# Optimization experiments

Measured on AMD Instinct MI355X. Metric: run time of the kernel, lower is better.

Reference implementation:

```python
import jax, jax.numpy as jnp
import numpy as np

C_IN = 64
C_INT = 32

def conv1x1(x, w, b):
    # x: [B,C,H,W], w: [O,C], b: [O]
    return jnp.einsum('bchw,oc->bohw', x, w) + b[None, :, None, None]

def maxpool2(x):
    # 2x2 max pool, stride 2. x: [B,C,H,W]
    B, C, H, W = x.shape
    return x.reshape(B, C, H // 2, 2, W // 2, 2).max(axis=(3, 5))

def setup_inputs() -> dict:
    key = jax.random.key(0)
    ks = jax.random.split(key, 9)
    s = 1.0 / np.sqrt(C_IN)
    si = 1.0 / np.sqrt(C_INT)
    x = jax.random.normal(ks[0], (16, C_IN, 64, 64), dtype=jnp.float32)
    return {
        'x': x,
        'w_origin': jax.random.normal(ks[1], (C_INT, C_IN), dtype=jnp.float32) * s,
        'b_origin': jax.random.normal(ks[2], (C_INT,), dtype=jnp.float32) * s,
        'w_theta': jax.random.normal(ks[3], (C_INT, C_IN), dtype=jnp.float32) * s,
        'b_theta': jax.random.normal(ks[4], (C_INT,), dtype=jnp.float32) * s,
        'w_phi': jax.random.normal(ks[5], (C_INT, C_IN), dtype=jnp.float32) * s,
        'b_phi': jax.random.normal(ks[6], (C_INT,), dtype=jnp.float32) * s,
        'w_W': jax.random.normal(ks[7], (C_IN, C_INT), dtype=jnp.float32) * si,
        'b_W': jax.random.normal(ks[8], (C_IN,), dtype=jnp.float32) * si,
    }

def reference(x, w_origin, b_origin, w_theta, b_theta, w_phi, b_phi, w_W, b_W):
    B, C, H, W = x.shape
    # value: conv1x1 + maxpool -> [B, Ci, H/2, W/2] -> [B, Nkv, Ci]
    f_x = maxpool2(conv1x1(x, w_origin, b_origin))
    f_x = f_x.reshape(B, C_INT, -1).transpose(0, 2, 1)
    # query: conv1x1 (no pooling) -> [B, N, Ci]
    theta_x = conv1x1(x, w_theta, b_theta).reshape(B, C_INT, -1).transpose(0, 2, 1)
    # key: conv1x1 + maxpool -> [B, Ci, Nkv]
    phi_x = maxpool2(conv1x1(x, w_phi, b_phi)).reshape(B, C_INT, -1)
    # attention: [B, N, Nkv]
    f = jnp.einsum('bnc,bcm->bnm', theta_x, phi_x)
    f_div_C = jax.nn.softmax(f, axis=-1)
    y = jnp.einsum('bnm,bmc->bnc', f_div_C, f_x)  # [B, N, Ci]
    y = y.transpose(0, 2, 1).reshape(B, C_INT, H, W)
    z = conv1x1(y, w_W, b_W) + x
    return z
```

## Files before the change

kernel.cpp:

```cpp
#include <hip/hip_runtime.h>
#include <math.h>


#define B_SZ 16
#define HW 4096
#define NKV 1024
#define XSTR 65
#define YS 40
#define LOG2E 1.4426950408889634f

typedef __attribute__((ext_vector_type(8))) short bfrag;
typedef __attribute__((ext_vector_type(4))) short sfrag;
typedef __attribute__((ext_vector_type(4))) float f32x4;

static __device__ __forceinline__ ushort f2bf(float v) {
  union { float f; uint u; } c; c.f = v;
  uint b = c.u + 0x7FFFu + ((c.u >> 16) & 1u);
  return (ushort)(b >> 16);
}
static __device__ __forceinline__ float bf2f(ushort h) {
  union { uint u; float f; } c; c.u = (uint)h << 16; return c.f;
}

__global__ __launch_bounds__(512) void k_qkv(
    const float* __restrict__ x,
    const float* __restrict__ wt, const float* __restrict__ bt,
    const float* __restrict__ wp, const float* __restrict__ bp,
    const float* __restrict__ wo, const float* __restrict__ bo,
    ushort* __restrict__ QH, ushort* __restrict__ QL,
    ushort* __restrict__ KH, ushort* __restrict__ KL, ushort* __restrict__ VF) {
  __shared__ float sx[128 * XSTR];
  __shared__ float sPool[2][2][32][33];

  int t = threadIdx.x;
  int W = t >> 6, lane = t & 63, l15 = lane & 15, quad = lane >> 4;
  int bb = blockIdx.x >> 5, rg = blockIdx.x & 31;
  int p0 = rg * 128;

  #pragma unroll
  for (int i = 0; i < 4; ++i) {
    int f = i * 512 + t;
    int c = f >> 5, u = f & 31;
    float4 v = *(const float4*)(x + ((size_t)bb << 18) + (size_t)c * HW + p0 + 4 * u);
    sx[(4*u+0) * XSTR + c] = v.x;
    sx[(4*u+1) * XSTR + c] = v.y;
    sx[(4*u+2) * XSTR + c] = v.z;
    sx[(4*u+3) * XSTR + c] = v.w;
  }
  __syncthreads();

  int pix = W * 16 + l15;
  bfrag xh[2], xl[2];
  #pragma unroll
  for (int kh2 = 0; kh2 < 2; ++kh2)
    #pragma unroll
    for (int j = 0; j < 8; ++j) {
      float v = sx[pix * XSTR + kh2 * 32 + quad * 8 + j];
      ushort hb = f2bf(v);
      xh[kh2][j] = (short)hb;
      xl[kh2][j] = (short)f2bf(v - bf2f(hb));
    }
  __syncthreads();

  f32x4 acc[2];

  acc[0] = (f32x4){0.f,0.f,0.f,0.f}; acc[1] = (f32x4){0.f,0.f,0.f,0.f};
  #pragma unroll
  for (int kh2 = 0; kh2 < 2; ++kh2)
    #pragma unroll
    for (int nt = 0; nt < 2; ++nt) {
      bfrag wh, wl;
      const float* wrow = wt + (size_t)(nt * 16 + l15) * 64 + kh2 * 32 + quad * 8;
      #pragma unroll
      for (int j = 0; j < 8; ++j) {
        float v = wrow[j] * LOG2E;
        ushort hb = f2bf(v);
        wh[j] = (short)hb; wl[j] = (short)f2bf(v - bf2f(hb));
      }
      acc[nt] = __builtin_amdgcn_mfma_f32_16x16x32_bf16(xh[kh2], wh, acc[nt], 0, 0, 0);
      acc[nt] = __builtin_amdgcn_mfma_f32_16x16x32_bf16(xl[kh2], wh, acc[nt], 0, 0, 0);
      acc[nt] = __builtin_amdgcn_mfma_f32_16x16x32_bf16(xh[kh2], wl, acc[nt], 0, 0, 0);
    }
  #pragma unroll
  for (int nt = 0; nt < 2; ++nt) {
    float bias = bt[nt * 16 + l15] * LOG2E;
    #pragma unroll
    for (int r = 0; r < 4; ++r)
      sx[(W * 16 + quad * 4 + r) * XSTR + nt * 16 + l15] = acc[nt][r] + bias;
  }

  int prow = (W * 16 + quad * 4) >> 6;
  int px2  = ((W * 16 + quad * 4) & 63) >> 1;

  acc[0] = (f32x4){0.f,0.f,0.f,0.f}; acc[1] = (f32x4){0.f,0.f,0.f,0.f};
  #pragma unroll
  for (int kh2 = 0; kh2 < 2; ++kh2)
    #pragma unroll
    for (int nt = 0; nt < 2; ++nt) {
      bfrag wh, wl;
      const float* wrow = wp + (size_t)(nt * 16 + l15) * 64 + kh2 * 32 + quad * 8;
      #pragma unroll
      for (int j = 0; j < 8; ++j) {
        float v = wrow[j];
        ushort hb = f2bf(v);
        wh[j] = (short)hb; wl[j] = (short)f2bf(v - bf2f(hb));
      }
      acc[nt] = __builtin_amdgcn_mfma_f32_16x16x32_bf16(xh[kh2], wh, acc[nt], 0, 0, 0);
      acc[nt] = __builtin_amdgcn_mfma_f32_16x16x32_bf16(xl[kh2], wh, acc[nt], 0, 0, 0);
      acc[nt] = __builtin_amdgcn_mfma_f32_16x16x32_bf16(xh[kh2], wl, acc[nt], 0, 0, 0);
    }
  #pragma unroll
  for (int nt = 0; nt < 2; ++nt) {
    float bias = bp[nt * 16 + l15];
    sPool[0][prow][px2    ][nt * 16 + l15] = fmaxf(acc[nt][0], acc[nt][1]) + bias;
    sPool[0][prow][px2 + 1][nt * 16 + l15] = fmaxf(acc[nt][2], acc[nt][3]) + bias;
  }

  acc[0] = (f32x4){0.f,0.f,0.f,0.f}; acc[1] = (f32x4){0.f,0.f,0.f,0.f};
  #pragma unroll
  for (int kh2 = 0; kh2 < 2; ++kh2)
    #pragma unroll
    for (int nt = 0; nt < 2; ++nt) {
      bfrag wh;
      const float* wrow = wo + (size_t)(nt * 16 + l15) * 64 + kh2 * 32 + quad * 8;
      #pragma unroll
      for (int j = 0; j < 8; ++j) wh[j] = (short)f2bf(wrow[j]);
      acc[nt] = __builtin_amdgcn_mfma_f32_16x16x32_bf16(xh[kh2], wh, acc[nt], 0, 0, 0);
      acc[nt] = __builtin_amdgcn_mfma_f32_16x16x32_bf16(xl[kh2], wh, acc[nt], 0, 0, 0);
    }
  #pragma unroll
  for (int nt = 0; nt < 2; ++nt) {
    float bias = bo[nt * 16 + l15];
    sPool[1][prow][px2    ][nt * 16 + l15] = fmaxf(acc[nt][0], acc[nt][1]) + bias;
    sPool[1][prow][px2 + 1][nt * 16 + l15] = fmaxf(acc[nt][2], acc[nt][3]) + bias;
  }
  __syncthreads();

  {
    int qt = t >> 6, ln = t & 63, fl = ln & 15, fq = ln >> 4;
    union { ushort u[8]; uint4 v; } Hh, Ll;
    #pragma unroll
    for (int j = 0; j < 8; ++j) {
      float v = sx[(qt * 16 + fl) * XSTR + fq * 8 + j];
      ushort hb = f2bf(v);
      Hh.u[j] = hb;
      Ll.u[j] = f2bf(v - bf2f(hb));
    }
    size_t base = ((size_t)(bb * 256 + rg * 8 + qt) * 64 + ln) * 8;
    *(uint4*)(QH + base) = Hh.v;
    *(uint4*)(QL + base) = Ll.v;
  }

  #pragma unroll
  for (int f = t; f < 1024; f += 512) {
    int tt = f >> 9, rem = f & 511;
    int ln = rem >> 3, j = rem & 7;
    int kvl = tt * 16 + (ln & 15);
    int ch = (ln >> 4) * 8 + j;
    float v = fmaxf(sPool[0][0][kvl][ch], sPool[0][1][kvl][ch]);
    ushort hb = f2bf(v);
    size_t base = ((size_t)(bb * 64 + rg * 2 + tt) * 64 + ln) * 8 + j;
    KH[base] = hb;
    KL[base] = f2bf(v - bf2f(hb));
  }

  #pragma unroll
  for (int f = t; f < 1024; f += 512) {
    int tt = f >> 9, mt = (f >> 8) & 1;
    int ln = (f >> 2) & 63, j = f & 3;
    int kvl = tt * 16 + ((ln >> 4) << 2) + j;
    int ch = mt * 16 + (ln & 15);
    float v = fmaxf(sPool[1][0][kvl][ch], sPool[1][1][kvl][ch]);
    VF[(((size_t)(bb * 64 + rg * 2 + tt) * 2 + mt) * 64 + ln) * 4 + j] = f2bf(v);
  }
}

__global__ __launch_bounds__(256, 4) void k_attn(
    const ushort* __restrict__ QH, const ushort* __restrict__ QL,
    const ushort* __restrict__ KH, const ushort* __restrict__ KL,
    const ushort* __restrict__ VF,
    const float* __restrict__ x, const float* __restrict__ wW,
    const float* __restrict__ bW, float* __restrict__ z) {
  __shared__ float smem[4 * 64 * 36 + 4 * 64];
  float* mrg = smem;
  float* sS  = smem + 4 * 64 * 36;

  int t = threadIdx.x;
  int w = t >> 6, lane = t & 63, l15 = lane & 15, quad = lane >> 4;
  int bb = blockIdx.x >> 6;
  int bq = blockIdx.x & 63;

  bfrag qh[4], ql[4];
  #pragma unroll
  for (int qt = 0; qt < 4; ++qt) {
    size_t base = ((size_t)(bb * 256 + bq * 4 + qt) * 64 + lane) * 8;
    qh[qt] = *(const bfrag*)(QH + base);
    ql[qt] = *(const bfrag*)(QL + base);
  }

  const ushort* KHb = KH + (size_t)bb * 64 * 64 * 8;
  const ushort* KLb = KL + (size_t)bb * 64 * 64 * 8;
  const ushort* VFb = VF + (size_t)bb * 64 * 2 * 64 * 4;

  f32x4 accO[4][2];
  float spart[4] = {0.f, 0.f, 0.f, 0.f};
  #pragma unroll
  for (int qt = 0; qt < 4; ++qt) {
    accO[qt][0] = (f32x4){0.f,0.f,0.f,0.f};
    accO[qt][1] = (f32x4){0.f,0.f,0.f,0.f};
  }

  bfrag kh[2], kl[2];
  sfrag vf[2][2];
  auto loadT = [&](int buf, int i) {
    int gt = w * 16 + i;
    size_t kb = ((size_t)gt * 64 + lane) * 8;
    kh[buf] = *(const bfrag*)(KHb + kb);
    kl[buf] = *(const bfrag*)(KLb + kb);
    vf[buf][0] = *(const sfrag*)(VFb + (((size_t)gt * 2 + 0) * 64 + lane) * 4);
    vf[buf][1] = *(const sfrag*)(VFb + (((size_t)gt * 2 + 1) * 64 + lane) * 4);
  };

  loadT(0, 0);
  #pragma unroll 2
  for (int i = 0; i < 16; ++i) {
    int cur = i & 1;
    if (i < 15) loadT(cur ^ 1, i + 1);
    #pragma unroll
    for (int qt = 0; qt < 4; ++qt) {
      f32x4 s = (f32x4){0.f,0.f,0.f,0.f};
      s = __builtin_amdgcn_mfma_f32_16x16x32_bf16(kh[cur], qh[qt], s, 0, 0, 0);
      s = __builtin_amdgcn_mfma_f32_16x16x32_bf16(kh[cur], ql[qt], s, 0, 0, 0);
      s = __builtin_amdgcn_mfma_f32_16x16x32_bf16(kl[cur], qh[qt], s, 0, 0, 0);
      float e0 = exp2f(s[0]), e1 = exp2f(s[1]);
      float e2 = exp2f(s[2]), e3 = exp2f(s[3]);
      spart[qt] += (e0 + e1) + (e2 + e3);
      union { uint2 u; sfrag s4; } pk;
      pk.u.x = (__float_as_uint(e0) >> 16) | (__float_as_uint(e1) & 0xFFFF0000u);
      pk.u.y = (__float_as_uint(e2) >> 16) | (__float_as_uint(e3) & 0xFFFF0000u);
      accO[qt][0] = __builtin_amdgcn_mfma_f32_16x16x16bf16_1k(vf[cur][0], pk.s4, accO[qt][0], 0, 0, 0);
      accO[qt][1] = __builtin_amdgcn_mfma_f32_16x16x16bf16_1k(vf[cur][1], pk.s4, accO[qt][1], 0, 0, 0);
    }
  }

  #pragma unroll
  for (int qt = 0; qt < 4; ++qt) {
    spart[qt] += __shfl_xor(spart[qt], 16);
    spart[qt] += __shfl_xor(spart[qt], 32);
  }

  #pragma unroll
  for (int qt = 0; qt < 4; ++qt) {
    #pragma unroll
    for (int mt = 0; mt < 2; ++mt)
      *(float4*)&mrg[((size_t)w * 64 + qt * 16 + l15) * 36 + mt * 16 + quad * 4] =
          make_float4(accO[qt][mt][0], accO[qt][mt][1], accO[qt][mt][2], accO[qt][mt][3]);
    if (lane < 16) sS[w * 64 + qt * 16 + l15] = spart[qt];
  }
  __syncthreads();

  int rq = t >> 2, rc = (t & 3) * 8;
  float yv[8];
  {
    float ssum = sS[rq] + sS[64 + rq] + sS[128 + rq] + sS[192 + rq];
    float inv = 1.0f / ssum;
    #pragma unroll
    for (int h = 0; h < 2; ++h) {
      float4 a = *(const float4*)&mrg[(size_t)rq * 36 + rc + 4 * h];
      float4 b = *(const float4*)&mrg[(size_t)(64 + rq) * 36 + rc + 4 * h];
      float4 c = *(const float4*)&mrg[(size_t)(128 + rq) * 36 + rc + 4 * h];
      float4 d = *(const float4*)&mrg[(size_t)(192 + rq) * 36 + rc + 4 * h];
      yv[4*h+0] = (a.x + b.x + c.x + d.x) * inv;
      yv[4*h+1] = (a.y + b.y + c.y + d.y) * inv;
      yv[4*h+2] = (a.z + b.z + c.z + d.z) * inv;
      yv[4*h+3] = (a.w + b.w + c.w + d.w) * inv;
    }
  }
  __syncthreads();

  ushort* yH = (ushort*)mrg;
  ushort* yL = yH + 64 * YS;
  {
    union { ushort u[8]; uint4 v; } Hh, Ll;
    #pragma unroll
    for (int j = 0; j < 8; ++j) {
      ushort hb = f2bf(yv[j]);
      Hh.u[j] = hb;
      Ll.u[j] = f2bf(yv[j] - bf2f(hb));
    }
    *(uint4*)&yH[rq * YS + rc] = Hh.v;
    *(uint4*)&yL[rq * YS + rc] = Ll.v;
  }
  __syncthreads();

  #pragma unroll
  for (int nt = 0; nt < 4; ++nt) {
    f32x4 d = (f32x4){0.f,0.f,0.f,0.f};
    #pragma unroll
    for (int kt = 0; kt < 2; ++kt) {
      float4 w4 = *(const float4*)&wW[(size_t)(w * 16 + l15) * 32 + kt * 16 + quad * 4];
      sfrag ah, al, yhf, ylf;
      #pragma unroll
      for (int j = 0; j < 4; ++j) {
        float v = (&w4.x)[j];
        ushort hb = f2bf(v);
        ah[j] = (short)hb; al[j] = (short)f2bf(v - bf2f(hb));
      }
      yhf = *(const sfrag*)&yH[(nt * 16 + l15) * YS + kt * 16 + quad * 4];
      ylf = *(const sfrag*)&yL[(nt * 16 + l15) * YS + kt * 16 + quad * 4];
      d = __builtin_amdgcn_mfma_f32_16x16x16bf16_1k(ah, yhf, d, 0, 0, 0);
      d = __builtin_amdgcn_mfma_f32_16x16x16bf16_1k(al, yhf, d, 0, 0, 0);
      d = __builtin_amdgcn_mfma_f32_16x16x16bf16_1k(ah, ylf, d, 0, 0, 0);
    }
    #pragma unroll
    for (int r = 0; r < 4; ++r) {
      int cout = w * 16 + quad * 4 + r;
      size_t zi = ((size_t)bb << 18) + ((size_t)cout << 12)
                + (size_t)(bq * 4 + nt) * 16 + l15;
      z[zi] = d[r] + bW[cout] + x[zi];
    }
  }
}

extern "C" void kernel_launch(void* const* d_in, const int* in_sizes, int n_in,
                              void* d_out, int out_size, void* d_ws, size_t ws_size,
                              hipStream_t stream) {
  const float* x   = (const float*)d_in[0];
  const float* w_o = (const float*)d_in[1];
  const float* b_o = (const float*)d_in[2];
  const float* w_t = (const float*)d_in[3];
  const float* b_t = (const float*)d_in[4];
  const float* w_p = (const float*)d_in[5];
  const float* b_p = (const float*)d_in[6];
  const float* w_W = (const float*)d_in[7];
  const float* b_W = (const float*)d_in[8];
  float* z = (float*)d_out;

  ushort* QH = (ushort*)d_ws;
  ushort* QL = QH + 2097152;
  ushort* KH = QL + 2097152;
  ushort* KL = KH + 524288;
  ushort* VF = KL + 524288;

  k_qkv<<<dim3(B_SZ * 32), dim3(512), 0, stream>>>(
      x, w_t, b_t, w_p, b_p, w_o, b_o, QH, QL, KH, KL, VF);
  k_attn<<<dim3(B_SZ * 64), dim3(256), 0, stream>>>(
      QH, QL, KH, KL, VF, x, w_W, b_W, z);
}
```

Before: 128.0 us.

## Fuse projection and attention kernels with per-batch spin barrier, keep Q in LDS

Merges the QKV projection kernel and the attention kernel into one launch. Each block now computes a 64-pixel tile's projections, writes K/V to global memory and keeps Q and the x tile in shared memory. Blocks then wait on a per-batch atomic counter spin barrier before running attention, and the residual add reads x from LDS. This removes the Q global round-trip, the second launch and the residual reload. In exchange it depends on all 64 blocks of a batch being co-resident, which risks deadlock otherwise. It also adds an extra memset and stores the per-wave partial outputs as bf16, which lowers accuracy.

After: 177.6 us. 38.7% more time.

```diff
diff --git a/kernel.cpp b/kernel.cpp
--- a/kernel.cpp
+++ b/kernel.cpp
@@ -4,9 +4,7 @@
 
 #define B_SZ 16
 #define HW 4096
-#define NKV 1024
-#define XSTR 65
-#define YS 40
+#define MST 40
 #define LOG2E 1.4426950408889634f
 
 typedef __attribute__((ext_vector_type(8))) short bfrag;
@@ -22,45 +20,54 @@
   union { uint u; float f; } c; c.u = (uint)h << 16; return c.f;
 }
 
-__global__ __launch_bounds__(512) void k_qkv(
+__global__ __launch_bounds__(256, 4) void k_fused(
     const float* __restrict__ x,
     const float* __restrict__ wt, const float* __restrict__ bt,
     const float* __restrict__ wp, const float* __restrict__ bp,
     const float* __restrict__ wo, const float* __restrict__ bo,
-    ushort* __restrict__ QH, ushort* __restrict__ QL,
-    ushort* __restrict__ KH, ushort* __restrict__ KL, ushort* __restrict__ VF) {
-  __shared__ float sx[128 * XSTR];
-  __shared__ float sPool[2][2][32][33];
+    const float* __restrict__ wW, const float* __restrict__ bW,
+    ushort* __restrict__ KH, ushort* __restrict__ KL, ushort* __restrict__ VF,
+    uint* __restrict__ ctr, float* __restrict__ z) {
+  __shared__ __align__(16) char smem_raw[16640 + 21504];
+  float*  sx    = (float*)smem_raw;
+  char*   reg2  = smem_raw + 16640;
+  float*  sQ    = (float*)reg2;
+  float*  sPool = (float*)(reg2 + 8448);
+  ushort* mrg   = (ushort*)reg2;
+  float*  sS    = (float*)(reg2 + 20480);
+  ushort* yH    = (ushort*)reg2;
+  ushort* yL    = yH + 64 * MST;
 
   int t = threadIdx.x;
-  int W = t >> 6, lane = t & 63, l15 = lane & 15, quad = lane >> 4;
-  int bb = blockIdx.x >> 5, rg = blockIdx.x & 31;
-  int p0 = rg * 128;
+  int w = t >> 6, lane = t & 63, l15 = lane & 15, quad = lane >> 4;
+  int b = blockIdx.x;
+  int bb = b >> 6, s = b & 63, r = s >> 1, j = s & 1;
+  const float* xb = x + ((size_t)bb << 18);
+  int grow0 = 2 * r, gcol0 = 32 * j;
 
   #pragma unroll
   for (int i = 0; i < 4; ++i) {
-    int f = i * 512 + t;
-    int c = f >> 5, u = f & 31;
-    float4 v = *(const float4*)(x + ((size_t)bb << 18) + (size_t)c * HW + p0 + 4 * u);
-    sx[(4*u+0) * XSTR + c] = v.x;
-    sx[(4*u+1) * XSTR + c] = v.y;
-    sx[(4*u+2) * XSTR + c] = v.z;
-    sx[(4*u+3) * XSTR + c] = v.w;
-  }
-  __syncthreads();
-
-  int pix = W * 16 + l15;
+    int f = i * 256 + t;
+    int ch = f >> 4, rem = f & 15, lrow = rem >> 3, c4 = rem & 7;
+    float4 v = *(const float4*)(xb + (size_t)ch * 4096
+                                   + (size_t)(grow0 + lrow) * 64 + gcol0 + c4 * 4);
+    int lp = lrow * 32 + c4 * 4;
+    sx[(lp+0)*65 + ch] = v.x; sx[(lp+1)*65 + ch] = v.y;
+    sx[(lp+2)*65 + ch] = v.z; sx[(lp+3)*65 + ch] = v.w;
+  }
+  __syncthreads();
+
+  int lpix = w * 16 + l15;
   bfrag xh[2], xl[2];
   #pragma unroll
   for (int kh2 = 0; kh2 < 2; ++kh2)
     #pragma unroll
-    for (int j = 0; j < 8; ++j) {
-      float v = sx[pix * XSTR + kh2 * 32 + quad * 8 + j];
+    for (int jj = 0; jj < 8; ++jj) {
+      float v = sx[lpix * 65 + kh2 * 32 + quad * 8 + jj];
       ushort hb = f2bf(v);
-      xh[kh2][j] = (short)hb;
-      xl[kh2][j] = (short)f2bf(v - bf2f(hb));
-    }
-  __syncthreads();
+      xh[kh2][jj] = (short)hb;
+      xl[kh2][jj] = (short)f2bf(v - bf2f(hb));
+    }
 
   f32x4 acc[2];
 
@@ -72,10 +79,10 @@
       bfrag wh, wl;
       const float* wrow = wt + (size_t)(nt * 16 + l15) * 64 + kh2 * 32 + quad * 8;
       #pragma unroll
-      for (int j = 0; j < 8; ++j) {
-        float v = wrow[j] * LOG2E;
+      for (int jj = 0; jj < 8; ++jj) {
+        float v = wrow[jj] * LOG2E;
         ushort hb = f2bf(v);
-        wh[j] = (short)hb; wl[j] = (short)f2bf(v - bf2f(hb));
+        wh[jj] = (short)hb; wl[jj] = (short)f2bf(v - bf2f(hb));
       }
       acc[nt] = __builtin_amdgcn_mfma_f32_16x16x32_bf16(xh[kh2], wh, acc[nt], 0, 0, 0);
       acc[nt] = __builtin_amdgcn_mfma_f32_16x16x32_bf16(xl[kh2], wh, acc[nt], 0, 0, 0);
@@ -85,12 +92,11 @@
   for (int nt = 0; nt < 2; ++nt) {
     float bias = bt[nt * 16 + l15] * LOG2E;
     #pragma unroll
-    for (int r = 0; r < 4; ++r)
-      sx[(W * 16 + quad * 4 + r) * XSTR + nt * 16 + l15] = acc[nt][r] + bias;
-  }
-
-  int prow = (W * 16 + quad * 4) >> 6;
-  int px2  = ((W * 16 + quad * 4) & 63) >> 1;
+    for (int rr = 0; rr < 4; ++rr)
+      sQ[(w * 16 + quad * 4 + rr) * 33 + nt * 16 + l15] = acc[nt][rr] + bias;
+  }
+
+  int hp = w * 8 + quad * 2;
 
   acc[0] = (f32x4){0.f,0.f,0.f,0.f}; acc[1] = (f32x4){0.f,0.f,0.f,0.f};
   #pragma unroll
@@ -100,10 +106,10 @@
       bfrag wh, wl;
       const float* wrow = wp + (size_t)(nt * 16 + l15) * 64 + kh2 * 32 + quad * 8;
       #pragma unroll
-      for (int j = 0; j < 8; ++j) {
-        float v = wrow[j];
+      for (int jj = 0; jj < 8; ++jj) {
+        float v = wrow[jj];
         ushort hb = f2bf(v);
-        wh[j] = (short)hb; wl[j] = (short)f2bf(v - bf2f(hb));
+        wh[jj] = (short)hb; wl[jj] = (short)f2bf(v - bf2f(hb));
       }
       acc[nt] = __builtin_amdgcn_mfma_f32_16x16x32_bf16(xh[kh2], wh, acc[nt], 0, 0, 0);
       acc[nt] = __builtin_amdgcn_mfma_f32_16x16x32_bf16(xl[kh2], wh, acc[nt], 0, 0, 0);
@@ -112,8 +118,8 @@
   #pragma unroll
   for (int nt = 0; nt < 2; ++nt) {
     float bias = bp[nt * 16 + l15];
-    sPool[0][prow][px2    ][nt * 16 + l15] = fmaxf(acc[nt][0], acc[nt][1]) + bias;
-    sPool[0][prow][px2 + 1][nt * 16 + l15] = fmaxf(acc[nt][2], acc[nt][3]) + bias;
+    sPool[(0 * 32 + hp    ) * 33 + nt * 16 + l15] = fmaxf(acc[nt][0], acc[nt][1]) + bias;
+    sPool[(0 * 32 + hp + 1) * 33 + nt * 16 + l15] = fmaxf(acc[nt][2], acc[nt][3]) + bias;
   }
 
   acc[0] = (f32x4){0.f,0.f,0.f,0.f}; acc[1] = (f32x4){0.f,0.f,0.f,0.f};
@@ -124,79 +130,60 @@
       bfrag wh;
       const float* wrow = wo + (size_t)(nt * 16 + l15) * 64 + kh2 * 32 + quad * 8;
       #pragma unroll
-      for (int j = 0; j < 8; ++j) wh[j] = (short)f2bf(wrow[j]);
+      for (int jj = 0; jj < 8; ++jj) wh[jj] = (short)f2bf(wrow[jj]);
       acc[nt] = __builtin_amdgcn_mfma_f32_16x16x32_bf16(xh[kh2], wh, acc[nt], 0, 0, 0);
       acc[nt] = __builtin_amdgcn_mfma_f32_16x16x32_bf16(xl[kh2], wh, acc[nt], 0, 0, 0);
     }
   #pragma unroll
   for (int nt = 0; nt < 2; ++nt) {
     float bias = bo[nt * 16 + l15];
-    sPool[1][prow][px2    ][nt * 16 + l15] = fmaxf(acc[nt][0], acc[nt][1]) + bias;
-    sPool[1][prow][px2 + 1][nt * 16 + l15] = fmaxf(acc[nt][2], acc[nt][3]) + bias;
-  }
-  __syncthreads();
-
-  {
-    int qt = t >> 6, ln = t & 63, fl = ln & 15, fq = ln >> 4;
-    union { ushort u[8]; uint4 v; } Hh, Ll;
-    #pragma unroll
-    for (int j = 0; j < 8; ++j) {
-      float v = sx[(qt * 16 + fl) * XSTR + fq * 8 + j];
-      ushort hb = f2bf(v);
-      Hh.u[j] = hb;
-      Ll.u[j] = f2bf(v - bf2f(hb));
-    }
-    size_t base = ((size_t)(bb * 256 + rg * 8 + qt) * 64 + ln) * 8;
-    *(uint4*)(QH + base) = Hh.v;
-    *(uint4*)(QL + base) = Ll.v;
-  }
-
-  #pragma unroll
-  for (int f = t; f < 1024; f += 512) {
-    int tt = f >> 9, rem = f & 511;
-    int ln = rem >> 3, j = rem & 7;
-    int kvl = tt * 16 + (ln & 15);
-    int ch = (ln >> 4) * 8 + j;
-    float v = fmaxf(sPool[0][0][kvl][ch], sPool[0][1][kvl][ch]);
+    sPool[(1 * 32 + hp    ) * 33 + nt * 16 + l15] = fmaxf(acc[nt][0], acc[nt][1]) + bias;
+    sPool[(1 * 32 + hp + 1) * 33 + nt * 16 + l15] = fmaxf(acc[nt][2], acc[nt][3]) + bias;
+  }
+  __syncthreads();
+
+  int tile = bb * 64 + s;
+  #pragma unroll
+  for (int f = t; f < 512; f += 256) {
+    int ln = f >> 3, ji = f & 7;
+    int kv = ln & 15, ch = (ln >> 4) * 8 + ji;
+    float v = fmaxf(sPool[(0 * 32 + kv) * 33 + ch], sPool[(0 * 32 + 16 + kv) * 33 + ch]);
     ushort hb = f2bf(v);
-    size_t base = ((size_t)(bb * 64 + rg * 2 + tt) * 64 + ln) * 8 + j;
+    size_t base = ((size_t)tile * 64 + ln) * 8 + ji;
     KH[base] = hb;
     KL[base] = f2bf(v - bf2f(hb));
   }
-
-  #pragma unroll
-  for (int f = t; f < 1024; f += 512) {
-    int tt = f >> 9, mt = (f >> 8) & 1;
-    int ln = (f >> 2) & 63, j = f & 3;
-    int kvl = tt * 16 + ((ln >> 4) << 2) + j;
-    int ch = mt * 16 + (ln & 15);
-    float v = fmaxf(sPool[1][0][kvl][ch], sPool[1][1][kvl][ch]);
-    VF[(((size_t)(bb * 64 + rg * 2 + tt) * 2 + mt) * 64 + ln) * 4 + j] = f2bf(v);
-  }
-}
-
-__global__ __launch_bounds__(256, 4) void k_attn(
-    const ushort* __restrict__ QH, const ushort* __restrict__ QL,
-    const ushort* __restrict__ KH, const ushort* __restrict__ KL,
-    const ushort* __restrict__ VF,
-    const float* __restrict__ x, const float* __restrict__ wW,
-    const float* __restrict__ bW, float* __restrict__ z) {
-  __shared__ float smem[4 * 64 * 36 + 4 * 64];
-  float* mrg = smem;
-  float* sS  = smem + 4 * 64 * 36;
-
-  int t = threadIdx.x;
-  int w = t >> 6, lane = t & 63, l15 = lane & 15, quad = lane >> 4;
-  int bb = blockIdx.x >> 6;
-  int bq = blockIdx.x & 63;
+  #pragma unroll
+  for (int f = t; f < 512; f += 256) {
+    int mt = f >> 8, ln = (f >> 2) & 63, jv = f & 3;
+    int kv = ((ln >> 4) << 2) + jv, ch = mt * 16 + (ln & 15);
+    float v = fmaxf(sPool[(1 * 32 + kv) * 33 + ch], sPool[(1 * 32 + 16 + kv) * 33 + ch]);
+    VF[(((size_t)tile * 2 + mt) * 64 + ln) * 4 + jv] = f2bf(v);
+  }
+
+  __syncthreads();
+  if (t == 0) {
+    uint* cb = ctr + bb * 16;
+    __threadfence();
+    atomicAdd(cb, 1u);
+    int it = 0;
+    while (atomicAdd(cb, 0u) < 64u && ++it < (1 << 26))
+      __builtin_amdgcn_s_sleep(4);
+    __threadfence();
+  }
+  __syncthreads();
 
   bfrag qh[4], ql[4];
   #pragma unroll
-  for (int qt = 0; qt < 4; ++qt) {
-    size_t base = ((size_t)(bb * 256 + bq * 4 + qt) * 64 + lane) * 8;
-    qh[qt] = *(const bfrag*)(QH + base);
-    ql[qt] = *(const bfrag*)(QL + base);
-  }
+  for (int qt = 0; qt < 4; ++qt)
+    #pragma unroll
+    for (int jj = 0; jj < 8; ++jj) {
+      float v = sQ[(qt * 16 + l15) * 33 + quad * 8 + jj];
+      ushort hb = f2bf(v);
+      qh[qt][jj] = (short)hb;
+      ql[qt][jj] = (short)f2bf(v - bf2f(hb));
+    }
+  __syncthreads();
 
   const ushort* KHb = KH + (size_t)bb * 64 * 64 * 8;
   const ushort* KLb = KL + (size_t)bb * 64 * 64 * 8;
@@ -228,12 +215,12 @@
     if (i < 15) loadT(cur ^ 1, i + 1);
     #pragma unroll
     for (int qt = 0; qt < 4; ++qt) {
-      f32x4 s = (f32x4){0.f,0.f,0.f,0.f};
-      s = __builtin_amdgcn_mfma_f32_16x16x32_bf16(kh[cur], qh[qt], s, 0, 0, 0);
-      s = __builtin_amdgcn_mfma_f32_16x16x32_bf16(kh[cur], ql[qt], s, 0, 0, 0);
-      s = __builtin_amdgcn_mfma_f32_16x16x32_bf16(kl[cur], qh[qt], s, 0, 0, 0);
-      float e0 = exp2f(s[0]), e1 = exp2f(s[1]);
-      float e2 = exp2f(s[2]), e3 = exp2f(s[3]);
+      f32x4 sv = (f32x4){0.f,0.f,0.f,0.f};
+      sv = __builtin_amdgcn_mfma_f32_16x16x32_bf16(kh[cur], qh[qt], sv, 0, 0, 0);
+      sv = __builtin_amdgcn_mfma_f32_16x16x32_bf16(kh[cur], ql[qt], sv, 0, 0, 0);
+      sv = __builtin_amdgcn_mfma_f32_16x16x32_bf16(kl[cur], qh[qt], sv, 0, 0, 0);
+      float e0 = exp2f(sv[0]), e1 = exp2f(sv[1]);
+      float e2 = exp2f(sv[2]), e3 = exp2f(sv[3]);
       spart[qt] += (e0 + e1) + (e2 + e3);
       union { uint2 u; sfrag s4; } pk;
       pk.u.x = (__float_as_uint(e0) >> 16) | (__float_as_uint(e1) & 0xFFFF0000u);
@@ -248,13 +235,14 @@
     spart[qt] += __shfl_xor(spart[qt], 16);
     spart[qt] += __shfl_xor(spart[qt], 32);
   }
-
   #pragma unroll
   for (int qt = 0; qt < 4; ++qt) {
     #pragma unroll
     for (int mt = 0; mt < 2; ++mt)
-      *(float4*)&mrg[((size_t)w * 64 + qt * 16 + l15) * 36 + mt * 16 + quad * 4] =
-          make_float4(accO[qt][mt][0], accO[qt][mt][1], accO[qt][mt][2], accO[qt][mt][3]);
+      #pragma unroll
+      for (int rr = 0; rr < 4; ++rr)
+        mrg[(w * 64 + qt * 16 + l15) * MST + mt * 16 + quad * 4 + rr] =
+            f2bf(accO[qt][mt][rr]);
     if (lane < 16) sS[w * 64 + qt * 16 + l15] = spart[qt];
   }
   __syncthreads();
@@ -265,31 +253,26 @@
     float ssum = sS[rq] + sS[64 + rq] + sS[128 + rq] + sS[192 + rq];
     float inv = 1.0f / ssum;
     #pragma unroll
-    for (int h = 0; h < 2; ++h) {
-      float4 a = *(const float4*)&mrg[(size_t)rq * 36 + rc + 4 * h];
-      float4 b = *(const float4*)&mrg[(size_t)(64 + rq) * 36 + rc + 4 * h];
-      float4 c = *(const float4*)&mrg[(size_t)(128 + rq) * 36 + rc + 4 * h];
-      float4 d = *(const float4*)&mrg[(size_t)(192 + rq) * 36 + rc + 4 * h];
-      yv[4*h+0] = (a.x + b.x + c.x + d.x) * inv;
-      yv[4*h+1] = (a.y + b.y + c.y + d.y) * inv;
-      yv[4*h+2] = (a.z + b.z + c.z + d.z) * inv;
-      yv[4*h+3] = (a.w + b.w + c.w + d.w) * inv;
-    }
-  }
-  __syncthreads();
-
-  ushort* yH = (ushort*)mrg;
-  ushort* yL = yH + 64 * YS;
+    for (int jj = 0; jj < 8; ++jj) {
+      float acc8 = bf2f(mrg[(size_t)rq * MST + rc + jj])
+                 + bf2f(mrg[(size_t)(64 + rq) * MST + rc + jj])
+                 + bf2f(mrg[(size_t)(128 + rq) * MST + rc + jj])
+                 + bf2f(mrg[(size_t)(192 + rq) * MST + rc + jj]);
+      yv[jj] = acc8 * inv;
+    }
+  }
+  __syncthreads();
+
   {
-    union { ushort u[8]; uint4 v; } Hh, Ll;
-    #pragma unroll
-    for (int j = 0; j < 8; ++j) {
-      ushort hb = f2bf(yv[j]);
-      Hh.u[j] = hb;
-      Ll.u[j] = f2bf(yv[j] - bf2f(hb));
-    }
-    *(uint4*)&yH[rq * YS + rc] = Hh.v;
-    *(uint4*)&yL[rq * YS + rc] = Ll.v;
+    union { ushort u[8]; uint4 v4; } Hh, Ll;
+    #pragma unroll
+    for (int jj = 0; jj < 8; ++jj) {
+      ushort hb = f2bf(yv[jj]);
+      Hh.u[jj] = hb;
+      Ll.u[jj] = f2bf(yv[jj] - bf2f(hb));
+    }
+    *(uint4*)&yH[rq * MST + rc] = Hh.v4;
+    *(uint4*)&yL[rq * MST + rc] = Ll.v4;
   }
   __syncthreads();
 
@@ -301,23 +284,25 @@
       float4 w4 = *(const float4*)&wW[(size_t)(w * 16 + l15) * 32 + kt * 16 + quad * 4];
       sfrag ah, al, yhf, ylf;
       #pragma unroll
-      for (int j = 0; j < 4; ++j) {
-        float v = (&w4.x)[j];
+      for (int jj = 0; jj < 4; ++jj) {
+        float v = (&w4.x)[jj];
         ushort hb = f2bf(v);
-        ah[j] = (short)hb; al[j] = (short)f2bf(v - bf2f(hb));
+        ah[jj] = (short)hb; al[jj] = (short)f2bf(v - bf2f(hb));
       }
-      yhf = *(const sfrag*)&yH[(nt * 16 + l15) * YS + kt * 16 + quad * 4];
-      ylf = *(const sfrag*)&yL[(nt * 16 + l15) * YS + kt * 16 + quad * 4];
+      yhf = *(const sfrag*)&yH[(nt * 16 + l15) * MST + kt * 16 + quad * 4];
+      ylf = *(const sfrag*)&yL[(nt * 16 + l15) * MST + kt * 16 + quad * 4];
       d = __builtin_amdgcn_mfma_f32_16x16x16bf16_1k(ah, yhf, d, 0, 0, 0);
       d = __builtin_amdgcn_mfma_f32_16x16x16bf16_1k(al, yhf, d, 0, 0, 0);
       d = __builtin_amdgcn_mfma_f32_16x16x16bf16_1k(ah, ylf, d, 0, 0, 0);
     }
     #pragma unroll
-    for (int r = 0; r < 4; ++r) {
-      int cout = w * 16 + quad * 4 + r;
+    for (int rr = 0; rr < 4; ++rr) {
+      int cout = w * 16 + quad * 4 + rr;
+      int lp = nt * 16 + l15;
+      float xres = sx[lp * 65 + cout];
       size_t zi = ((size_t)bb << 18) + ((size_t)cout << 12)
-                + (size_t)(bq * 4 + nt) * 16 + l15;
-      z[zi] = d[r] + bW[cout] + x[zi];
+                + (size_t)(grow0 + (lp >> 5)) * 64 + gcol0 + (lp & 31);
+      z[zi] = d[rr] + bW[cout] + xres;
     }
   }
 }
@@ -336,14 +321,12 @@
   const float* b_W = (const float*)d_in[8];
   float* z = (float*)d_out;
 
-  ushort* QH = (ushort*)d_ws;
-  ushort* QL = QH + 2097152;
-  ushort* KH = QL + 2097152;
-  ushort* KL = KH + 524288;
-  ushort* VF = KL + 524288;
-
-  k_qkv<<<dim3(B_SZ * 32), dim3(512), 0, stream>>>(
-      x, w_t, b_t, w_p, b_p, w_o, b_o, QH, QL, KH, KL, VF);
-  k_attn<<<dim3(B_SZ * 64), dim3(256), 0, stream>>>(
-      QH, QL, KH, KL, VF, x, w_W, b_W, z);
+  uint*   ctr = (uint*)d_ws;
+  ushort* KH  = (ushort*)((char*)d_ws + 1024);
+  ushort* KL  = KH + 524288;
+  ushort* VF  = KL + 524288;
+
+  hipMemsetAsync(d_ws, 0, 1024, stream);
+  k_fused<<<dim3(1024), dim3(256), 0, stream>>>(
+      x, w_t, b_t, w_p, b_p, w_o, b_o, w_W, b_W, KH, KL, VF, ctr, z);
 }
```
